# Performance work log

Hardware: AMD Instinct MI355X
Metric: run time of the kernel (lower is better)

## Reference

```python
import jax, jax.numpy as jnp
import numpy as np
from jax import lax

G0, G1 = 16, 16
UNITS = 256


def setup_inputs() -> dict:
    key = jax.random.key(0)
    ks = jax.random.split(key, 20)
    B, H, W, C = 64, 512, 512, 3
    U = UNITS
    flat = 12 * 12 * 3  # after two VALID 3x3 convs on 16x16x3
    inp = {
        'image': jax.random.normal(ks[0], (B, H, W, C), jnp.float32),
        'section': jax.random.uniform(ks[1], (B, 3), jnp.float32),
        'h0': jax.random.normal(ks[2], (B, U), jnp.float32) * 0.1,
        'c0': jax.random.normal(ks[3], (B, U), jnp.float32) * 0.1,
        'conv1_k': jax.random.normal(ks[4], (3, 3, C, 3), jnp.float32) * 0.2,
        'conv1_b': jnp.zeros((3,), jnp.float32),
        'conv2_k': jax.random.normal(ks[5], (3, 3, 3, 3), jnp.float32) * 0.2,
        'conv2_b': jnp.zeros((3,), jnp.float32),
        'dense_w': jax.random.normal(ks[6], (flat, U), jnp.float32) * (1.0 / np.sqrt(flat)),
        'dense_b': jnp.zeros((U,), jnp.float32),
        'lstm_k': jax.random.normal(ks[7], (U, 4 * U), jnp.float32) * (1.0 / np.sqrt(U)),
        'lstm_rk': jax.random.normal(ks[8], (U, 4 * U), jnp.float32) * (1.0 / np.sqrt(U)),
        'lstm_b': jnp.zeros((4 * U,), jnp.float32),
        'nsc_w1': jax.random.normal(ks[9], (U, U), jnp.float32) * (1.0 / np.sqrt(U)),
        'nsc_b1': jnp.zeros((U,), jnp.float32),
        'nsc_w2': jax.random.normal(ks[10], (U, 3), jnp.float32) * (1.0 / np.sqrt(U)),
        'nsc_b2': jnp.zeros((3,), jnp.float32),
    }
    return inp


def _interpolate(image, section):
    # image: (B,H,W,C); section: (B,3) = (x, y, scale); coords in [0,1],
    # mapped linearly onto grid indices with constant (clamp) extension,
    # matching tfp.math.batch_interp_regular_nd_grid over image axes 1,2.
    B, H, W, C = image.shape
    starts = section[:, :2]                       # (B,2)
    stops = section[:, :2] + section[:, 2:]       # (B,2) broadcast scale
    t0 = jnp.linspace(0.0, 1.0, G0)               # along grid_dim[0]
    alpha = jnp.linspace(0.0, 1.0, G1)            # along grid_dim[1]
    # p0[b,i,j]: coordinate mapped to image axis 1 (H)
    p0 = (starts[:, 0, None] + t0[None, :] * (stops[:, 0] - starts[:, 0])[:, None])[:, :, None]
    p0 = jnp.broadcast_to(p0, (B, G0, G1))
    # p1[b,i,j]: coordinate mapped to image axis 2 (W)
    p1 = (starts[:, 1, None] + alpha[None, :] * (stops[:, 1] - starts[:, 1])[:, None])[:, None, :]
    p1 = jnp.broadcast_to(p1, (B, G0, G1))
    fy = jnp.clip(p0 * (H - 1), 0.0, H - 1)
    fx = jnp.clip(p1 * (W - 1), 0.0, W - 1)
    y0 = jnp.floor(fy).astype(jnp.int32)
    x0 = jnp.floor(fx).astype(jnp.int32)
    y1 = jnp.minimum(y0 + 1, H - 1)
    x1 = jnp.minimum(x0 + 1, W - 1)
    wy = (fy - y0)[..., None]
    wx = (fx - x0)[..., None]
    b = jnp.arange(B)[:, None, None]
    v00 = image[b, y0, x0]
    v01 = image[b, y0, x1]
    v10 = image[b, y1, x0]
    v11 = image[b, y1, x1]
    top = v00 * (1 - wx) + v01 * wx
    bot = v10 * (1 - wx) + v11 * wx
    return top * (1 - wy) + bot * wy            # (B,G0,G1,C)


def _conv_relu(x, k, b):
    y = lax.conv_general_dilated(x, k, (1, 1), 'VALID',
                                 dimension_numbers=('NHWC', 'HWIO', 'NHWC'))
    return jax.nn.relu(y + b)


def reference(image, section, h0, c0, conv1_k, conv1_b, conv2_k, conv2_b,
              dense_w, dense_b, lstm_k, lstm_rk, lstm_b,
              nsc_w1, nsc_b1, nsc_w2, nsc_b2):
    sec = _interpolate(image, section)                 # (B,16,16,C)
    x = _conv_relu(sec, conv1_k, conv1_b)              # (B,14,14,3)
    x = _conv_relu(x, conv2_k, conv2_b)                # (B,12,12,3)
    x = x.reshape(x.shape[0], -1)                      # (B,432)
    x = jax.nn.relu(x @ dense_w + dense_b)             # (B,U)
    # Keras LSTMCell: gate order i, f, g(c), o
    z = x @ lstm_k + h0 @ lstm_rk + lstm_b
    i, f, g, o = jnp.split(z, 4, axis=-1)
    c_new = jax.nn.sigmoid(f) * c0 + jax.nn.sigmoid(i) * jnp.tanh(g)
    h_new = jax.nn.sigmoid(o) * jnp.tanh(c_new)
    nsc = jax.nn.relu(h_new @ nsc_w1 + nsc_b1)
    next_section = jax.nn.sigmoid(nsc @ nsc_w2 + nsc_b2)  # (B,3)
    return h_new, c_new, next_section
```

## Files before the change

kernel.cpp:

```cpp
#include <hip/hip_runtime.h>
#include <math.h>

#define BATCH 64
#define IMH 512
#define IMW 512
#define UNITS 256

__device__ __forceinline__ float sigmoidf_(float x) {
    return 1.0f / (1.0f + __expf(-x));
}
__device__ __forceinline__ float tanhf_(float x) {
    float e = __expf(2.0f * x);
    return 1.0f - 2.0f / (e + 1.0f);
}

__global__ __launch_bounds__(256) void fused_cell_kernel(
    const float* __restrict__ image,
    const float* __restrict__ section,
    const float* __restrict__ h0,
    const float* __restrict__ c0,
    const float* __restrict__ k1,
    const float* __restrict__ b1,
    const float* __restrict__ k2,
    const float* __restrict__ b2,
    const float* __restrict__ dw,
    const float* __restrict__ db,
    const float* __restrict__ lk,
    const float* __restrict__ lrk,
    const float* __restrict__ lb,
    const float* __restrict__ w1,
    const float* __restrict__ nb1,
    const float* __restrict__ w2,
    const float* __restrict__ nb2,
    float* __restrict__ out)
{
    const int b   = blockIdx.x;
    const int tid = threadIdx.x;

    __shared__ float s_sec[16][16][3];
    __shared__ float s_c1[14][14][3];
    __shared__ float s_flat[432];
    __shared__ float s_x[256];
    __shared__ float s_h0[256];
    __shared__ float s_hn[256];
    __shared__ float s_nsc[256];
    __shared__ float s_k1[84];
    __shared__ float s_k2[84];

    if (tid < 81)       s_k1[tid]      = k1[tid];
    else if (tid < 84)  s_k1[tid]      = b1[tid - 81];
    else if (tid < 165) s_k2[tid - 84] = k2[tid - 84];
    else if (tid < 168) s_k2[tid - 84] = b2[tid - 165];
    s_h0[tid] = h0[b * UNITS + tid];

    {
        const float s0 = section[b * 3 + 0];
        const float s1 = section[b * 3 + 1];
        const float s2 = section[b * 3 + 2];
        const int i = tid >> 4, j = tid & 15;
        float p0 = s0 + (float)i * (1.0f / 15.0f) * s2;
        float p1 = s1 + (float)j * (1.0f / 15.0f) * s2;
        float fy = fminf(fmaxf(p0 * 511.0f, 0.0f), 511.0f);
        float fx = fminf(fmaxf(p1 * 511.0f, 0.0f), 511.0f);
        int y0 = (int)floorf(fy);
        int x0 = (int)floorf(fx);
        int y1 = min(y0 + 1, 511);
        int x1 = min(x0 + 1, 511);
        float wy = fy - (float)y0;
        float wx = fx - (float)x0;
        const float* base = image + (size_t)b * IMH * IMW * 3;
        const float* p00 = base + (y0 * IMW + x0) * 3;
        const float* p01 = base + (y0 * IMW + x1) * 3;
        const float* p10 = base + (y1 * IMW + x0) * 3;
        const float* p11 = base + (y1 * IMW + x1) * 3;
        #pragma unroll
        for (int c = 0; c < 3; ++c) {
            float top = p00[c] * (1.0f - wx) + p01[c] * wx;
            float bot = p10[c] * (1.0f - wx) + p11[c] * wx;
            s_sec[i][j][c] = top * (1.0f - wy) + bot * wy;
        }
    }
    __syncthreads();

    if (tid < 196) {
        const int i = tid / 14, j = tid % 14;
        float a0 = s_k1[81], a1 = s_k1[82], a2 = s_k1[83];
        #pragma unroll
        for (int di = 0; di < 3; ++di)
            #pragma unroll
            for (int dj = 0; dj < 3; ++dj)
                #pragma unroll
                for (int ci = 0; ci < 3; ++ci) {
                    float v = s_sec[i + di][j + dj][ci];
                    const int kb = ((di * 3 + dj) * 3 + ci) * 3;
                    a0 += v * s_k1[kb + 0];
                    a1 += v * s_k1[kb + 1];
                    a2 += v * s_k1[kb + 2];
                }
        s_c1[i][j][0] = fmaxf(a0, 0.0f);
        s_c1[i][j][1] = fmaxf(a1, 0.0f);
        s_c1[i][j][2] = fmaxf(a2, 0.0f);
    }
    __syncthreads();

    if (tid < 144) {
        const int i = tid / 12, j = tid % 12;
        float a0 = s_k2[81], a1 = s_k2[82], a2 = s_k2[83];
        #pragma unroll
        for (int di = 0; di < 3; ++di)
            #pragma unroll
            for (int dj = 0; dj < 3; ++dj)
                #pragma unroll
                for (int ci = 0; ci < 3; ++ci) {
                    float v = s_c1[i + di][j + dj][ci];
                    const int kb = ((di * 3 + dj) * 3 + ci) * 3;
                    a0 += v * s_k2[kb + 0];
                    a1 += v * s_k2[kb + 1];
                    a2 += v * s_k2[kb + 2];
                }
        const int fb = tid * 3;
        s_flat[fb + 0] = fmaxf(a0, 0.0f);
        s_flat[fb + 1] = fmaxf(a1, 0.0f);
        s_flat[fb + 2] = fmaxf(a2, 0.0f);
    }
    __syncthreads();

    {
        float acc = db[tid];
        #pragma unroll 4
        for (int k = 0; k < 432; ++k)
            acc += s_flat[k] * dw[k * 256 + tid];
        s_x[tid] = fmaxf(acc, 0.0f);
    }
    __syncthreads();

    {
        float zi = lb[tid];
        float zf = lb[256 + tid];
        float zg = lb[512 + tid];
        float zo = lb[768 + tid];
        #pragma unroll 4
        for (int k = 0; k < 256; ++k) {
            const float xv = s_x[k];
            const float hv = s_h0[k];
            const float* lkr = lk  + k * 1024 + tid;
            const float* lrr = lrk + k * 1024 + tid;
            zi += xv * lkr[0]   + hv * lrr[0];
            zf += xv * lkr[256] + hv * lrr[256];
            zg += xv * lkr[512] + hv * lrr[512];
            zo += xv * lkr[768] + hv * lrr[768];
        }
        const float cprev = c0[b * UNITS + tid];
        const float cn = sigmoidf_(zf) * cprev + sigmoidf_(zi) * tanhf_(zg);
        const float hn = sigmoidf_(zo) * tanhf_(cn);
        out[b * UNITS + tid] = hn;
        out[BATCH * UNITS + b * UNITS + tid] = cn;
        s_hn[tid] = hn;
    }
    __syncthreads();

    {
        float acc = nb1[tid];
        #pragma unroll 4
        for (int k = 0; k < 256; ++k)
            acc += s_hn[k] * w1[k * 256 + tid];
        s_nsc[tid] = fmaxf(acc, 0.0f);
    }
    __syncthreads();

    if (tid < 192) {
        const int j = tid >> 6;
        const int l = tid & 63;
        float p = 0.0f;
        #pragma unroll
        for (int k = l; k < 256; k += 64)
            p += s_nsc[k] * w2[k * 3 + j];
        #pragma unroll
        for (int off = 32; off > 0; off >>= 1)
            p += __shfl_down(p, off);
        if (l == 0)
            out[2 * BATCH * UNITS + b * 3 + j] = sigmoidf_(p + nb2[j]);
    }
}

extern "C" void kernel_launch(void* const* d_in, const int* in_sizes, int n_in,
                              void* d_out, int out_size, void* d_ws, size_t ws_size,
                              hipStream_t stream) {
    const float* image   = (const float*)d_in[0];
    const float* section = (const float*)d_in[1];
    const float* h0      = (const float*)d_in[2];
    const float* c0      = (const float*)d_in[3];
    const float* k1      = (const float*)d_in[4];
    const float* b1      = (const float*)d_in[5];
    const float* k2      = (const float*)d_in[6];
    const float* b2      = (const float*)d_in[7];
    const float* dw      = (const float*)d_in[8];
    const float* db      = (const float*)d_in[9];
    const float* lk      = (const float*)d_in[10];
    const float* lrk     = (const float*)d_in[11];
    const float* lb      = (const float*)d_in[12];
    const float* w1      = (const float*)d_in[13];
    const float* nb1     = (const float*)d_in[14];
    const float* w2      = (const float*)d_in[15];
    const float* nb2     = (const float*)d_in[16];
    float* out = (float*)d_out;

    fused_cell_kernel<<<BATCH, 256, 0, stream>>>(
        image, section, h0, c0, k1, b1, k2, b2, dw, db,
        lk, lrk, lb, w1, nb1, w2, nb2, out);
}
```

Baseline: 369.0 us.

## Widen blocks to 1024 threads and split dense/LSTM matvecs across thread groups

Launches 1024 threads per batch block instead of 256. The dense and nsc matvecs split their reduction dimension into four groups, with partial sums combined in shared memory. The LSTM matvec gives each thread one of the 1024 gate columns instead of four. The aim is more memory-level parallelism on the weight streaming, since with only 64 blocks the GPU is badly underfilled. The cost is extra barriers, shared-memory partial-sum buffers, and idle threads during the early conv stages.

```diff
diff --git a/kernel.cpp b/kernel.cpp
--- a/kernel.cpp
+++ b/kernel.cpp
@@ -14,7 +14,7 @@
     return 1.0f - 2.0f / (e + 1.0f);
 }
 
-__global__ __launch_bounds__(256) void fused_cell_kernel(
+__global__ __launch_bounds__(1024) void fused_cell_kernel(
     const float* __restrict__ image,
     const float* __restrict__ section,
     const float* __restrict__ h0,
@@ -44,6 +44,8 @@
     __shared__ float s_h0[256];
     __shared__ float s_hn[256];
     __shared__ float s_nsc[256];
+    __shared__ float s_z[1024];
+    __shared__ float s_part[4][256];
     __shared__ float s_k1[84];
     __shared__ float s_k2[84];
 
@@ -51,9 +53,9 @@
     else if (tid < 84)  s_k1[tid]      = b1[tid - 81];
     else if (tid < 165) s_k2[tid - 84] = k2[tid - 84];
     else if (tid < 168) s_k2[tid - 84] = b2[tid - 165];
-    s_h0[tid] = h0[b * UNITS + tid];
-
-    {
+    if (tid < 256) s_h0[tid] = h0[b * UNITS + tid];
+
+    if (tid < 256) {
         const float s0 = section[b * 3 + 0];
         const float s1 = section[b * 3 + 1];
         const float s2 = section[b * 3 + 2];
@@ -126,30 +128,36 @@
     __syncthreads();
 
     {
-        float acc = db[tid];
-        #pragma unroll 4
-        for (int k = 0; k < 432; ++k)
-            acc += s_flat[k] * dw[k * 256 + tid];
-        s_x[tid] = fmaxf(acc, 0.0f);
-    }
+        const int g = tid >> 8, col = tid & 255;
+        const float* wp = dw + (g * 108) * 256 + col;
+        const float* fp = s_flat + g * 108;
+        float acc = 0.0f;
+        #pragma unroll 6
+        for (int k = 0; k < 108; ++k)
+            acc += fp[k] * wp[k * 256];
+        s_part[g][col] = acc;
+    }
+    __syncthreads();
+    if (tid < 256)
+        s_x[tid] = fmaxf(s_part[0][tid] + s_part[1][tid] + s_part[2][tid] +
+                         s_part[3][tid] + db[tid], 0.0f);
     __syncthreads();
 
     {
-        float zi = lb[tid];
-        float zf = lb[256 + tid];
-        float zg = lb[512 + tid];
-        float zo = lb[768 + tid];
-        #pragma unroll 4
-        for (int k = 0; k < 256; ++k) {
-            const float xv = s_x[k];
-            const float hv = s_h0[k];
-            const float* lkr = lk  + k * 1024 + tid;
-            const float* lrr = lrk + k * 1024 + tid;
-            zi += xv * lkr[0]   + hv * lrr[0];
-            zf += xv * lkr[256] + hv * lrr[256];
-            zg += xv * lkr[512] + hv * lrr[512];
-            zo += xv * lkr[768] + hv * lrr[768];
-        }
+        float z = lb[tid];
+        const float* lkp = lk  + tid;
+        const float* lrp = lrk + tid;
+        #pragma unroll 8
+        for (int k = 0; k < 256; ++k)
+            z += s_x[k] * lkp[k * 1024] + s_h0[k] * lrp[k * 1024];
+        s_z[tid] = z;
+    }
+    __syncthreads();
+    if (tid < 256) {
+        const float zi = s_z[tid];
+        const float zf = s_z[256 + tid];
+        const float zg = s_z[512 + tid];
+        const float zo = s_z[768 + tid];
         const float cprev = c0[b * UNITS + tid];
         const float cn = sigmoidf_(zf) * cprev + sigmoidf_(zi) * tanhf_(zg);
         const float hn = sigmoidf_(zo) * tanhf_(cn);
@@ -160,12 +168,19 @@
     __syncthreads();
 
     {
-        float acc = nb1[tid];
-        #pragma unroll 4
-        for (int k = 0; k < 256; ++k)
-            acc += s_hn[k] * w1[k * 256 + tid];
-        s_nsc[tid] = fmaxf(acc, 0.0f);
-    }
+        const int g = tid >> 8, col = tid & 255;
+        const float* wp = w1 + (g * 64) * 256 + col;
+        const float* hp = s_hn + g * 64;
+        float acc = 0.0f;
+        #pragma unroll 8
+        for (int k = 0; k < 64; ++k)
+            acc += hp[k] * wp[k * 256];
+        s_part[g][col] = acc;
+    }
+    __syncthreads();
+    if (tid < 256)
+        s_nsc[tid] = fmaxf(s_part[0][tid] + s_part[1][tid] + s_part[2][tid] +
+                           s_part[3][tid] + nb1[tid], 0.0f);
     __syncthreads();
 
     if (tid < 192) {
@@ -205,7 +220,7 @@
     const float* nb2     = (const float*)d_in[16];
     float* out = (float*)d_out;
 
-    fused_cell_kernel<<<BATCH, 256, 0, stream>>>(
+    fused_cell_kernel<<<BATCH, 1024, 0, stream>>>(
         image, section, h0, c0, k1, b1, k2, b2, dw, db,
         lk, lrk, lb, w1, nb1, w2, nb2, out);
 }
```

Measured after the change: 299.6 us, median of 2. 18.8% less time.
